# Kernel tuning notes

Hardware: AMD Instinct MI355X
Metric: run time of the kernel (lower is better)

## Reference

```python
import jax, jax.numpy as jnp
import numpy as np

N = 131072
IN_C1 = 64
MED_C = 64
OUT_C = 64
EPS = 1e-8


def _glorot(key, shape):
    fan_in = shape[0]
    bound = 1.0 / np.sqrt(fan_in)
    return jax.random.uniform(key, shape, jnp.float32, -bound, bound)


def setup_inputs() -> dict:
    key = jax.random.key(0)
    ks = jax.random.split(key, 16)
    inp = {
        "key_value_input": jax.random.normal(ks[0], (N, IN_C1), jnp.float32),
        "query_input": jax.random.normal(ks[1], (N, 7), jnp.float32),
        # Linear params stored as [in, out] (y = x @ W + b)
        "key_W": _glorot(ks[2], (IN_C1, MED_C)), "key_b": jnp.zeros((MED_C,), jnp.float32),
        "value_W": _glorot(ks[3], (IN_C1, MED_C)), "value_b": jnp.zeros((MED_C,), jnp.float32),
        "T_W": _glorot(ks[4], (7, MED_C * MED_C)), "T_b": jnp.zeros((MED_C * MED_C,), jnp.float32),
        "d1_W": _glorot(ks[5], (MED_C, 64)), "d1_b": jnp.zeros((64,), jnp.float32),
        "d2_W": _glorot(ks[6], (64, 32)), "d2_b": jnp.zeros((32,), jnp.float32),
        "d3_W": _glorot(ks[7], (32, OUT_C)), "d3_b": jnp.zeros((OUT_C,), jnp.float32),
        "scale": jnp.float32(1.0),
    }
    return inp


def reference(key_value_input, query_input, key_W, key_b, value_W, value_b,
              T_W, T_b, d1_W, d1_b, d2_W, d2_b, d3_W, d3_b, scale):
    # Per-token hypernetwork: T [N, med_c, med_c]
    T = (query_input @ T_W + T_b).reshape(-1, MED_C, MED_C)
    k = key_value_input @ key_W + key_b              # [N, med_c]
    v = key_value_input @ value_W + value_b          # [N, med_c]
    # query = T @ kv  (batched mat-vec)
    q = jnp.einsum('nij,nj->ni', T, key_value_input)  # [N, med_c]
    att = q * k
    # F.normalize(p=2, dim=-1, eps=1e-8): x / max(||x||_2, eps)
    norm = jnp.linalg.norm(att, axis=-1, keepdims=True)
    att = att / jnp.maximum(norm, EPS)
    v = jax.nn.softmax(v * scale, axis=-1)
    x = att * v
    # small MLP head d
    h = jax.nn.relu(x @ d1_W + d1_b)
    h = jax.nn.relu(h @ d2_W + d2_b)
    return h @ d3_W + d3_b
```

## Files before the change

kernel.cpp:

```cpp
#include <hip/hip_runtime.h>
#include <math.h>

typedef _Float16 f16_t;
typedef __attribute__((ext_vector_type(8))) _Float16 f16x8;
typedef __attribute__((ext_vector_type(4))) float f32x4;

#define NTOK 131072
#define MT   256
#define TPB  256
#define RP16 72
#define OP32 68
#define SLABB 9216

#define OFF_KEY 0
#define OFF_VAL 4096
#define OFF_T   8192
#define OFF_D1  40960
#define OFF_D2  45056
#define OFF_D3  47104
#define WTOT    49152

__device__ __forceinline__ f32x4 mfma1(f16x8 a, f16x8 b, f32x4 c) {
    return __builtin_amdgcn_mfma_f32_16x16x32_f16(a, b, c, 0, 0, 0);
}

struct B2 { f16x8 b0, b1; };

__device__ __forceinline__ B2 loadB_lds(const f16_t* __restrict__ b, int c, int l15, int quad) {
    const char* base = (const char*)b;
    int o0 = (16 * c + l15) * 128 + quad * 16;
    int sw = (l15 & 7) << 4;
    B2 r;
    r.b0 = *(const f16x8*)(base + (o0 ^ sw));
    r.b1 = *(const f16x8*)(base + ((o0 + 64) ^ sw));
    return r;
}

#define GEMML(buf, c, a00, a01, a10, a11, acc0, acc1) do {        \
    B2 Bf = loadB_lds((buf), (c), l15, quad);                      \
    acc0 = mfma1(a01, Bf.b1, mfma1(a00, Bf.b0, acc0));             \
    acc1 = mfma1(a11, Bf.b1, mfma1(a10, Bf.b0, acc1));             \
} while (0)

#define TCOL(tb, c, QA0, QA1, QA2, QA3, Q0, Q1, Q2, Q3) do {       \
    B2 Bf = loadB_lds((tb), (c), l15, quad);                        \
    f32x4 z = {};                                                   \
    f32x4 tt0 = mfma1(ah01, Bf.b1, mfma1(ah00, Bf.b0, z));          \
    Q0 += QA0 * tt0;                                                \
    f32x4 tt1 = mfma1(ah11, Bf.b1, mfma1(ah10, Bf.b0, z));          \
    Q1 += QA1 * tt1;                                                \
    f32x4 tt2 = mfma1(ah21, Bf.b1, mfma1(ah20, Bf.b0, z));          \
    Q2 += QA2 * tt2;                                                \
    f32x4 tt3 = mfma1(ah31, Bf.b1, mfma1(ah30, Bf.b0, z));          \
    Q3 += QA3 * tt3;                                                \
} while (0)

__device__ __forceinline__ void gl_lds16(const void* g, void* l) {
    __builtin_amdgcn_global_load_lds(
        (const __attribute__((address_space(1))) unsigned int*)g,
        (__attribute__((address_space(3))) unsigned int*)l, 16, 0, 0);
}

__device__ __forceinline__ void stage8k(const f16_t* __restrict__ gsrc, f16_t* lbuf, int tid) {
#pragma unroll
    for (int i = 0; i < 2; ++i) {
        int o = (i * 256 + tid) * 16;
        int g = o ^ (((o >> 7) & 7) << 4);
        gl_lds16((const char*)gsrc + g, (char*)lbuf + (o & ~1023));
    }
}
__device__ __forceinline__ void stage4k_r128(const f16_t* __restrict__ gsrc, f16_t* lbuf, int tid) {
    int o = tid * 16;
    int g = o ^ (((o >> 7) & 7) << 4);
    gl_lds16((const char*)gsrc + g, (char*)lbuf + (o & ~1023));
}
__device__ __forceinline__ void stage4k_r64(const f16_t* __restrict__ gsrc, f16_t* lbuf, int tid) {
    int o = tid * 16;
    int g = o ^ (((o >> 7) & 3) << 4);
    gl_lds16((const char*)gsrc + g, (char*)lbuf + (o & ~1023));
}

#define VMW2() asm volatile("s_waitcnt vmcnt(2)" ::: "memory")
#define VMW0() asm volatile("s_waitcnt vmcnt(0)" ::: "memory")
#define BAR()  do { __builtin_amdgcn_s_barrier(); asm volatile("" ::: "memory"); } while (0)

__global__ __launch_bounds__(256)
void prep_w(const float* __restrict__ keyW, const float* __restrict__ valW,
            const float* __restrict__ TW,   const float* __restrict__ TB,
            const float* __restrict__ d1W,  const float* __restrict__ d2W,
            const float* __restrict__ d3W,  f16_t* __restrict__ wsf)
{
    int idx = blockIdx.x * 256 + threadIdx.x;
    if (idx >= WTOT) return;
    float src;
    if (idx < OFF_VAL) {
        int r = idx - OFF_KEY, n = r >> 6, j = r & 63;
        src = keyW[j * 64 + n];
    } else if (idx < OFF_T) {
        int r = idx - OFF_VAL, n = r >> 6, j = r & 63;
        src = valW[j * 64 + n];
    } else if (idx < OFF_D1) {
        int r = idx - OFF_T, p = r >> 12, q = r & 4095;
        src = (p < 7) ? TW[p * 4096 + q] : TB[q];
    } else if (idx < OFF_D2) {
        int r = idx - OFF_D1, n = r >> 6, j = r & 63;
        src = d1W[j * 64 + n];
    } else if (idx < OFF_D3) {
        int r = idx - OFF_D2, n = r >> 6, j = r & 63;
        src = d2W[j * 32 + n];
    } else {
        int r = idx - OFF_D3, n = r >> 5, j = r & 31;
        src = d3W[j * 64 + n];
    }
    wsf[idx] = (f16_t)src;
}

__device__ __forceinline__ void front_rt(
    f16_t* __restrict__ Rf,
    const f16_t* __restrict__ keyb, const f16_t* __restrict__ valb,
    int l15, int quad, int rtb,
    f16x8 a0, f16x8 a1,
    f32x4 q0, f32x4 q1, f32x4 q2, f32x4 q3,
    f32x4 kbv, f32x4 vbv, float sc)
{
    f32x4 k0 = {}, k1 = {}, k2 = {}, k3 = {}, v0 = {}, v1 = {}, v2 = {}, v3 = {};
    { B2 B = loadB_lds(keyb, 0, l15, quad); k0 = mfma1(a1, B.b1, mfma1(a0, B.b0, k0)); }
    { B2 B = loadB_lds(keyb, 1, l15, quad); k1 = mfma1(a1, B.b1, mfma1(a0, B.b0, k1)); }
    { B2 B = loadB_lds(keyb, 2, l15, quad); k2 = mfma1(a1, B.b1, mfma1(a0, B.b0, k2)); }
    { B2 B = loadB_lds(keyb, 3, l15, quad); k3 = mfma1(a1, B.b1, mfma1(a0, B.b0, k3)); }
    { B2 B = loadB_lds(valb, 0, l15, quad); v0 = mfma1(a1, B.b1, mfma1(a0, B.b0, v0)); }
    { B2 B = loadB_lds(valb, 1, l15, quad); v1 = mfma1(a1, B.b1, mfma1(a0, B.b0, v1)); }
    { B2 B = loadB_lds(valb, 2, l15, quad); v2 = mfma1(a1, B.b1, mfma1(a0, B.b0, v2)); }
    { B2 B = loadB_lds(valb, 3, l15, quad); v3 = mfma1(a1, B.b1, mfma1(a0, B.b0, v3)); }

    f32x4 sv0 = (v0 + vbv[0]) * sc;
    f32x4 sv1 = (v1 + vbv[1]) * sc;
    f32x4 sv2 = (v2 + vbv[2]) * sc;
    f32x4 sv3 = (v3 + vbv[3]) * sc;

    f32x4 mx;
#pragma unroll
    for (int e = 0; e < 4; ++e)
        mx[e] = fmaxf(fmaxf(sv0[e], sv1[e]), fmaxf(sv2[e], sv3[e]));
#pragma unroll
    for (int m = 1; m < 16; m <<= 1)
#pragma unroll
        for (int e = 0; e < 4; ++e) mx[e] = fmaxf(mx[e], __shfl_xor(mx[e], m, 64));
#pragma unroll
    for (int e = 0; e < 4; ++e) {
        sv0[e] = __expf(sv0[e] - mx[e]);
        sv1[e] = __expf(sv1[e] - mx[e]);
        sv2[e] = __expf(sv2[e] - mx[e]);
        sv3[e] = __expf(sv3[e] - mx[e]);
    }
    f32x4 se = sv0 + sv1 + sv2 + sv3;
#pragma unroll
    for (int m = 1; m < 16; m <<= 1)
#pragma unroll
        for (int e = 0; e < 4; ++e) se[e] += __shfl_xor(se[e], m, 64);

    f32x4 at0 = q0 * (k0 + kbv[0]);
    f32x4 at1 = q1 * (k1 + kbv[1]);
    f32x4 at2 = q2 * (k2 + kbv[2]);
    f32x4 at3 = q3 * (k3 + kbv[3]);
    f32x4 nr = at0 * at0 + at1 * at1 + at2 * at2 + at3 * at3;
#pragma unroll
    for (int m = 1; m < 16; m <<= 1)
#pragma unroll
        for (int e = 0; e < 4; ++e) nr[e] += __shfl_xor(nr[e], m, 64);

    f32x4 fac;
#pragma unroll
    for (int e = 0; e < 4; ++e)
        fac[e] = 1.0f / (fmaxf(sqrtf(nr[e]), 1e-8f) * se[e]);

#pragma unroll
    for (int e = 0; e < 4; ++e) {
        f16_t* rr = Rf + (rtb + quad * 4 + e) * RP16 + l15;
        rr[0]  = (f16_t)(at0[e] * sv0[e] * fac[e]);
        rr[16] = (f16_t)(at1[e] * sv1[e] * fac[e]);
        rr[32] = (f16_t)(at2[e] * sv2[e] * fac[e]);
        rr[48] = (f16_t)(at3[e] * sv3[e] * fac[e]);
    }
}

__device__ __forceinline__ void d1_rt(f16_t* __restrict__ Rf, const f16_t* __restrict__ wb,
                                      int l15, int quad, int rtb, f32x4 b1v)
{
    f16x8 x00 = *(const f16x8*)(Rf + (rtb + l15) * RP16 + quad * 8);
    f16x8 x01 = *(const f16x8*)(Rf + (rtb + l15) * RP16 + 32 + quad * 8);
    f16x8 x10 = *(const f16x8*)(Rf + (rtb + 16 + l15) * RP16 + quad * 8);
    f16x8 x11 = *(const f16x8*)(Rf + (rtb + 16 + l15) * RP16 + 32 + quad * 8);
    f32x4 h00 = {}, h01 = {}, h02 = {}, h03 = {};
    f32x4 h10 = {}, h11 = {}, h12 = {}, h13 = {};
    GEMML(wb, 0, x00, x01, x10, x11, h00, h10);
    GEMML(wb, 1, x00, x01, x10, x11, h01, h11);
    GEMML(wb, 2, x00, x01, x10, x11, h02, h12);
    GEMML(wb, 3, x00, x01, x10, x11, h03, h13);
#pragma unroll
    for (int e = 0; e < 4; ++e) {
        f16_t* r0 = Rf + (rtb + quad * 4 + e) * RP16 + l15;
        r0[0]  = (f16_t)fmaxf(h00[e] + b1v[0], 0.f);
        r0[16] = (f16_t)fmaxf(h01[e] + b1v[1], 0.f);
        r0[32] = (f16_t)fmaxf(h02[e] + b1v[2], 0.f);
        r0[48] = (f16_t)fmaxf(h03[e] + b1v[3], 0.f);
        f16_t* r1 = Rf + (rtb + 16 + quad * 4 + e) * RP16 + l15;
        r1[0]  = (f16_t)fmaxf(h10[e] + b1v[0], 0.f);
        r1[16] = (f16_t)fmaxf(h11[e] + b1v[1], 0.f);
        r1[32] = (f16_t)fmaxf(h12[e] + b1v[2], 0.f);
        r1[48] = (f16_t)fmaxf(h13[e] + b1v[3], 0.f);
    }
}

__device__ __forceinline__ void d2_rt(f16_t* __restrict__ Rf, const f16_t* __restrict__ wb,
                                      int l15, int quad, int rtb, float b20, float b21)
{
    f16x8 x00 = *(const f16x8*)(Rf + (rtb + l15) * RP16 + quad * 8);
    f16x8 x01 = *(const f16x8*)(Rf + (rtb + l15) * RP16 + 32 + quad * 8);
    f16x8 x10 = *(const f16x8*)(Rf + (rtb + 16 + l15) * RP16 + quad * 8);
    f16x8 x11 = *(const f16x8*)(Rf + (rtb + 16 + l15) * RP16 + 32 + quad * 8);
    f32x4 g00 = {}, g01 = {}, g10 = {}, g11 = {};
    GEMML(wb, 0, x00, x01, x10, x11, g00, g10);
    GEMML(wb, 1, x00, x01, x10, x11, g01, g11);
#pragma unroll
    for (int e = 0; e < 4; ++e) {
        f16_t* r0 = Rf + (rtb + quad * 4 + e) * RP16 + l15;
        r0[0]  = (f16_t)fmaxf(g00[e] + b20, 0.f);
        r0[16] = (f16_t)fmaxf(g01[e] + b21, 0.f);
        f16_t* r1 = Rf + (rtb + 16 + quad * 4 + e) * RP16 + l15;
        r1[0]  = (f16_t)fmaxf(g10[e] + b20, 0.f);
        r1[16] = (f16_t)fmaxf(g11[e] + b21, 0.f);
    }
}

__device__ __forceinline__ void d3_rt(f16_t* __restrict__ Rf, float* __restrict__ Of,
                                      const char* __restrict__ d3b,
                                      int l15, int quad, int lane, int rtb,
                                      f32x4 b3v, float* __restrict__ obase)
{
    f16x8 a30 = *(const f16x8*)(Rf + (rtb + l15) * RP16 + quad * 8);
    f16x8 a31 = *(const f16x8*)(Rf + (rtb + 16 + l15) * RP16 + quad * 8);
    const int sw3 = ((l15 >> 1) & 3) << 4;
#pragma unroll
    for (int h = 0; h < 2; ++h) {
        const f16x8 a3 = h ? a31 : a30;
#pragma unroll
        for (int c = 0; c < 4; ++c) {
            int o3 = (16 * c + l15) * 64 + quad * 16;
            f16x8 bw = *(const f16x8*)(d3b + (o3 ^ sw3));
            f32x4 z = {};
            f32x4 o = mfma1(a3, bw, z);
#pragma unroll
            for (int e = 0; e < 4; ++e)
                Of[(quad * 4 + e) * OP32 + 16 * c + l15] = o[e] + b3v[c];
        }
#pragma unroll
        for (int i = 0; i < 4; ++i) {
            const int r4 = i * 4 + quad;
            f32x4 v = *(const f32x4*)(Of + r4 * OP32 + l15 * 4);
            *(f32x4*)(obase + rtb * 64 + h * 1024 + i * 256 + lane * 4) = v;
        }
    }
}

__global__ __launch_bounds__(TPB, 2)
void fused_mfma(const float* __restrict__ kv_in, const float* __restrict__ q_in,
                const float* __restrict__ keyB,  const float* __restrict__ valB,
                const float* __restrict__ d1B,   const float* __restrict__ d2B,
                const float* __restrict__ d3B,   const float* __restrict__ scale_p,
                const f16_t* __restrict__ wsf,   float* __restrict__ out)
{
    __shared__ __align__(16) unsigned char Slab[4][SLABB];
    __shared__ __align__(16) float Qs[8][MT];
    __shared__ __align__(16) f16_t WB[2][4096];

    const int tid  = threadIdx.x;
    const int wv   = tid >> 6, lane = tid & 63;
    const int quad = lane >> 4, l15 = lane & 15;
    const int RB   = wv * 64;
    const long t0  = (long)blockIdx.x * MT;

    f16_t* __restrict__ Rf = (f16_t*)Slab[wv];
    float* __restrict__ Of = (float*)Slab[wv];

    stage8k(wsf + OFF_T + 0 * 4096, WB[0], tid);
    stage8k(wsf + OFF_T + 1 * 4096, WB[1], tid);

    f32x4 kbv, vbv, b1v, b3v;
#pragma unroll
    for (int c = 0; c < 4; ++c) {
        kbv[c] = keyB[16 * c + l15];  vbv[c] = valB[16 * c + l15];
        b1v[c] = d1B[16 * c + l15];   b3v[c] = d3B[16 * c + l15];
    }
    const float b20 = d2B[l15], b21 = d2B[16 + l15];
    const float sc = scale_p[0];

    {
        const int r = lane >> 1, half = lane & 1;
#pragma unroll
        for (int s = 0; s < 2; ++s) {
            const float4* p4 = (const float4*)(kv_in + (t0 + RB + s * 32 + r) * 64 + half * 32);
            f16_t* dst = Rf + (s * 32 + r) * RP16 + half * 32;
#pragma unroll
            for (int b = 0; b < 4; ++b) {
                float4 f0 = p4[2 * b], f1 = p4[2 * b + 1];
                f16x8 h;
                h[0] = (f16_t)f0.x; h[1] = (f16_t)f0.y; h[2] = (f16_t)f0.z; h[3] = (f16_t)f0.w;
                h[4] = (f16_t)f1.x; h[5] = (f16_t)f1.y; h[6] = (f16_t)f1.z; h[7] = (f16_t)f1.w;
                *(f16x8*)(dst + 8 * b) = h;
            }
        }
    }
    {
        const float* qp = q_in + (t0 + RB + lane) * 7;
#pragma unroll
        for (int p = 0; p < 7; ++p) Qs[p][RB + lane] = qp[p];
        Qs[7][RB + lane] = 1.0f;
    }

    f16x8 ah00 = *(const f16x8*)(Rf + l15 * RP16 + quad * 8);
    f16x8 ah01 = *(const f16x8*)(Rf + l15 * RP16 + 32 + quad * 8);
    f16x8 ah10 = *(const f16x8*)(Rf + (16 + l15) * RP16 + quad * 8);
    f16x8 ah11 = *(const f16x8*)(Rf + (16 + l15) * RP16 + 32 + quad * 8);
    f16x8 ah20 = *(const f16x8*)(Rf + (32 + l15) * RP16 + quad * 8);
    f16x8 ah21 = *(const f16x8*)(Rf + (32 + l15) * RP16 + 32 + quad * 8);
    f16x8 ah30 = *(const f16x8*)(Rf + (48 + l15) * RP16 + quad * 8);
    f16x8 ah31 = *(const f16x8*)(Rf + (48 + l15) * RP16 + 32 + quad * 8);

    f32x4 q00 = {}, q01 = {}, q02 = {}, q03 = {};
    f32x4 q10 = {}, q11 = {}, q12 = {}, q13 = {};
    f32x4 q20 = {}, q21 = {}, q22 = {}, q23 = {};
    f32x4 q30 = {}, q31 = {}, q32 = {}, q33 = {};
#pragma unroll 1
    for (int p = 0; p < 8; ++p) {
        const f16_t* tb = WB[p & 1];
        VMW2(); BAR();
        f32x4 qa0 = *(const f32x4*)&Qs[p][RB + quad * 4];
        f32x4 qa1 = *(const f32x4*)&Qs[p][RB + 16 + quad * 4];
        f32x4 qa2 = *(const f32x4*)&Qs[p][RB + 32 + quad * 4];
        f32x4 qa3 = *(const f32x4*)&Qs[p][RB + 48 + quad * 4];
        TCOL(tb, 0, qa0, qa1, qa2, qa3, q00, q10, q20, q30);
        TCOL(tb, 1, qa0, qa1, qa2, qa3, q01, q11, q21, q31);
        TCOL(tb, 2, qa0, qa1, qa2, qa3, q02, q12, q22, q32);
        TCOL(tb, 3, qa0, qa1, qa2, qa3, q03, q13, q23, q33);
        BAR();
        const f16_t* nsrc = (p < 6) ? (wsf + OFF_T + (p + 2) * 4096)
                                    : ((p == 6) ? (wsf + OFF_KEY) : (wsf + OFF_VAL));
        stage8k(nsrc, WB[p & 1], tid);
    }
    VMW0(); BAR();

    front_rt(Rf, WB[0], WB[1], l15, quad, 0,  ah00, ah01, q00, q01, q02, q03, kbv, vbv, sc);
    front_rt(Rf, WB[0], WB[1], l15, quad, 16, ah10, ah11, q10, q11, q12, q13, kbv, vbv, sc);
    front_rt(Rf, WB[0], WB[1], l15, quad, 32, ah20, ah21, q20, q21, q22, q23, kbv, vbv, sc);
    front_rt(Rf, WB[0], WB[1], l15, quad, 48, ah30, ah31, q30, q31, q32, q33, kbv, vbv, sc);
    BAR();
    stage8k(wsf + OFF_D1, WB[0], tid);
    stage4k_r128(wsf + OFF_D2, WB[1], tid);
    stage4k_r64 (wsf + OFF_D3, WB[1] + 2048, tid);
    VMW0(); BAR();

    d1_rt(Rf, WB[0], l15, quad, 0,  b1v);
    d1_rt(Rf, WB[0], l15, quad, 32, b1v);
    d2_rt(Rf, WB[1], l15, quad, 0,  b20, b21);
    d2_rt(Rf, WB[1], l15, quad, 32, b20, b21);

    float* __restrict__ obase = out + (t0 + RB) * 64;
    const char* d3b = (const char*)(&WB[1][2048]);
    d3_rt(Rf, Of, d3b, l15, quad, lane, 0,  b3v, obase);
    d3_rt(Rf, Of, d3b, l15, quad, lane, 32, b3v, obase);
}

extern "C" void kernel_launch(void* const* d_in, const int* in_sizes, int n_in,
                              void* d_out, int out_size, void* d_ws, size_t ws_size,
                              hipStream_t stream) {
    (void)in_sizes; (void)n_in; (void)out_size; (void)ws_size;
    const float* kv_in = (const float*)d_in[0];
    const float* q_in  = (const float*)d_in[1];
    const float* keyW  = (const float*)d_in[2];
    const float* keyB  = (const float*)d_in[3];
    const float* valW  = (const float*)d_in[4];
    const float* valB  = (const float*)d_in[5];
    const float* TW    = (const float*)d_in[6];
    const float* TB    = (const float*)d_in[7];
    const float* d1W   = (const float*)d_in[8];
    const float* d1B   = (const float*)d_in[9];
    const float* d2W   = (const float*)d_in[10];
    const float* d2B   = (const float*)d_in[11];
    const float* d3W   = (const float*)d_in[12];
    const float* d3B   = (const float*)d_in[13];
    const float* scale = (const float*)d_in[14];
    f16_t* wsf = (f16_t*)d_ws;
    float* outp = (float*)d_out;

    prep_w<<<(WTOT + 255) / 256, 256, 0, stream>>>(keyW, valW, TW, TB, d1W, d2W, d3W, wsf);
    fused_mfma<<<NTOK / MT, TPB, 0, stream>>>(kv_in, q_in, keyB, valB,
                                              d1B, d2B, d3B, scale, wsf, outp);
}
```

Measured before the change: 130.0 us.

## Triple-buffer weight staging to drop a barrier and use DPP row reductions

The double-buffered weight staging in the T-hypernetwork loop becomes a triple buffer. The next-next stage is now issued right after the single barrier, which removes the second per-iteration barrier. The d1 weights are also prefetched into a free buffer before the front stage, so they overlap with front_rt. The 16-lane shuffle reductions for softmax max/sum and the L2 norm are replaced with DPP row-level reductions, avoiding ds_swizzle/bpermute latency. The cost is 8KB more LDS per block, which may reduce occupancy at two blocks per CU.

```diff
diff --git a/kernel.cpp b/kernel.cpp
--- a/kernel.cpp
+++ b/kernel.cpp
@@ -22,6 +22,32 @@
 
 __device__ __forceinline__ f32x4 mfma1(f16x8 a, f16x8 b, f32x4 c) {
     return __builtin_amdgcn_mfma_f32_16x16x32_f16(a, b, c, 0, 0, 0);
+}
+
+#define DPPF(x, C) __int_as_float(__builtin_amdgcn_update_dpp( \
+    0, __float_as_int(x), (C), 0xF, 0xF, true))
+
+__device__ __forceinline__ void red16_sum4(f32x4& x) {
+#pragma unroll
+    for (int e = 0; e < 4; ++e) {
+        float v = x[e];
+        v += DPPF(v, 0xB1);
+        v += DPPF(v, 0x4E);
+        v += DPPF(v, 0x141);
+        v += DPPF(v, 0x140);
+        x[e] = v;
+    }
+}
+__device__ __forceinline__ void red16_max4(f32x4& x) {
+#pragma unroll
+    for (int e = 0; e < 4; ++e) {
+        float v = x[e];
+        v = fmaxf(v, DPPF(v, 0xB1));
+        v = fmaxf(v, DPPF(v, 0x4E));
+        v = fmaxf(v, DPPF(v, 0x141));
+        v = fmaxf(v, DPPF(v, 0x140));
+        x[e] = v;
+    }
 }
 
 struct B2 { f16x8 b0, b1; };
@@ -142,10 +168,7 @@
 #pragma unroll
     for (int e = 0; e < 4; ++e)
         mx[e] = fmaxf(fmaxf(sv0[e], sv1[e]), fmaxf(sv2[e], sv3[e]));
-#pragma unroll
-    for (int m = 1; m < 16; m <<= 1)
-#pragma unroll
-        for (int e = 0; e < 4; ++e) mx[e] = fmaxf(mx[e], __shfl_xor(mx[e], m, 64));
+    red16_max4(mx);
 #pragma unroll
     for (int e = 0; e < 4; ++e) {
         sv0[e] = __expf(sv0[e] - mx[e]);
@@ -154,20 +177,14 @@
         sv3[e] = __expf(sv3[e] - mx[e]);
     }
     f32x4 se = sv0 + sv1 + sv2 + sv3;
-#pragma unroll
-    for (int m = 1; m < 16; m <<= 1)
-#pragma unroll
-        for (int e = 0; e < 4; ++e) se[e] += __shfl_xor(se[e], m, 64);
+    red16_sum4(se);
 
     f32x4 at0 = q0 * (k0 + kbv[0]);
     f32x4 at1 = q1 * (k1 + kbv[1]);
     f32x4 at2 = q2 * (k2 + kbv[2]);
     f32x4 at3 = q3 * (k3 + kbv[3]);
     f32x4 nr = at0 * at0 + at1 * at1 + at2 * at2 + at3 * at3;
-#pragma unroll
-    for (int m = 1; m < 16; m <<= 1)
-#pragma unroll
-        for (int e = 0; e < 4; ++e) nr[e] += __shfl_xor(nr[e], m, 64);
+    red16_sum4(nr);
 
     f32x4 fac;
 #pragma unroll
@@ -272,7 +289,7 @@
 {
     __shared__ __align__(16) unsigned char Slab[4][SLABB];
     __shared__ __align__(16) float Qs[8][MT];
-    __shared__ __align__(16) f16_t WB[2][4096];
+    __shared__ __align__(16) f16_t WB[3][4096];
 
     const int tid  = threadIdx.x;
     const int wv   = tid >> 6, lane = tid & 63;
@@ -333,8 +350,11 @@
     f32x4 q30 = {}, q31 = {}, q32 = {}, q33 = {};
 #pragma unroll 1
     for (int p = 0; p < 8; ++p) {
-        const f16_t* tb = WB[p & 1];
+        const f16_t* tb = WB[p % 3];
         VMW2(); BAR();
+        const f16_t* nsrc = (p < 6) ? (wsf + OFF_T + (p + 2) * 4096)
+                                    : ((p == 6) ? (wsf + OFF_KEY) : (wsf + OFF_VAL));
+        stage8k(nsrc, WB[(p + 2) % 3], tid);
         f32x4 qa0 = *(const f32x4*)&Qs[p][RB + quad * 4];
         f32x4 qa1 = *(const f32x4*)&Qs[p][RB + 16 + quad * 4];
         f32x4 qa2 = *(const f32x4*)&Qs[p][RB + 32 + quad * 4];
@@ -343,30 +363,27 @@
         TCOL(tb, 1, qa0, qa1, qa2, qa3, q01, q11, q21, q31);
         TCOL(tb, 2, qa0, qa1, qa2, qa3, q02, q12, q22, q32);
         TCOL(tb, 3, qa0, qa1, qa2, qa3, q03, q13, q23, q33);
-        BAR();
-        const f16_t* nsrc = (p < 6) ? (wsf + OFF_T + (p + 2) * 4096)
-                                    : ((p == 6) ? (wsf + OFF_KEY) : (wsf + OFF_VAL));
-        stage8k(nsrc, WB[p & 1], tid);
     }
     VMW0(); BAR();
 
-    front_rt(Rf, WB[0], WB[1], l15, quad, 0,  ah00, ah01, q00, q01, q02, q03, kbv, vbv, sc);
-    front_rt(Rf, WB[0], WB[1], l15, quad, 16, ah10, ah11, q10, q11, q12, q13, kbv, vbv, sc);
-    front_rt(Rf, WB[0], WB[1], l15, quad, 32, ah20, ah21, q20, q21, q22, q23, kbv, vbv, sc);
-    front_rt(Rf, WB[0], WB[1], l15, quad, 48, ah30, ah31, q30, q31, q32, q33, kbv, vbv, sc);
+    stage8k(wsf + OFF_D1, WB[1], tid);
+
+    front_rt(Rf, WB[2], WB[0], l15, quad, 0,  ah00, ah01, q00, q01, q02, q03, kbv, vbv, sc);
+    front_rt(Rf, WB[2], WB[0], l15, quad, 16, ah10, ah11, q10, q11, q12, q13, kbv, vbv, sc);
+    front_rt(Rf, WB[2], WB[0], l15, quad, 32, ah20, ah21, q20, q21, q22, q23, kbv, vbv, sc);
+    front_rt(Rf, WB[2], WB[0], l15, quad, 48, ah30, ah31, q30, q31, q32, q33, kbv, vbv, sc);
     BAR();
-    stage8k(wsf + OFF_D1, WB[0], tid);
-    stage4k_r128(wsf + OFF_D2, WB[1], tid);
-    stage4k_r64 (wsf + OFF_D3, WB[1] + 2048, tid);
+    stage4k_r128(wsf + OFF_D2, WB[2], tid);
+    stage4k_r64 (wsf + OFF_D3, WB[2] + 2048, tid);
     VMW0(); BAR();
 
-    d1_rt(Rf, WB[0], l15, quad, 0,  b1v);
-    d1_rt(Rf, WB[0], l15, quad, 32, b1v);
-    d2_rt(Rf, WB[1], l15, quad, 0,  b20, b21);
-    d2_rt(Rf, WB[1], l15, quad, 32, b20, b21);
+    d1_rt(Rf, WB[1], l15, quad, 0,  b1v);
+    d1_rt(Rf, WB[1], l15, quad, 32, b1v);
+    d2_rt(Rf, WB[2], l15, quad, 0,  b20, b21);
+    d2_rt(Rf, WB[2], l15, quad, 32, b20, b21);
 
     float* __restrict__ obase = out + (t0 + RB) * 64;
-    const char* d3b = (const char*)(&WB[1][2048]);
+    const char* d3b = (const char*)(&WB[2][2048]);
     d3_rt(Rf, Of, d3b, l15, quad, lane, 0,  b3v, obase);
     d3_rt(Rf, Of, d3b, l15, quad, lane, 32, b3v, obase);
 }
```

New measurement: 132.0 us. About the same (+1.6%).
